# Optimization experiments

Measured on AMD Instinct MI355X. Metric: run time of the kernel, lower is better.

The kernel has to match this reference:

```python
import jax, jax.numpy as jnp
import numpy as np


def setup_inputs() -> dict:
    key = jax.random.key(0)
    k1, k2 = jax.random.split(key)
    latents = jax.random.normal(k1, (32, 1024, 64), dtype=jnp.float32)
    codebook = jax.random.normal(k2, (8192, 64), dtype=jnp.float32)
    return {"latents": latents, "codebook": codebook}


def reference(latents, codebook):
    # Faithful to: cdist(latents_flat, codebook) -> argmin(dim=1) -> reshape(B, L)
    B, L, D = latents.shape
    x = latents.reshape(-1, D)                         # (N, D)
    x2 = jnp.sum(x * x, axis=1, keepdims=True)         # (N, 1)
    c2 = jnp.sum(codebook * codebook, axis=1)          # (K,)
    # (N, K) distance matrix, then argmin reduction
    d2 = x2 - 2.0 * (x @ codebook.T) + c2[None, :]
    indices = jnp.argmin(d2, axis=1)                   # (N,)
    return indices.reshape(B, L)
```

## Files before the change

kernel.cpp:

```cpp
#include <hip/hip_runtime.h>
#include <stdint.h>


#define N_TOTAL 32768
#define K_CODES 8192
#define EPS_GAP 0.008f

typedef __attribute__((ext_vector_type(4)))  float  floatx4;
typedef __attribute__((ext_vector_type(8)))  __bf16 bf16x8;

#define O_C2    0u
#define O_CBSW  32768u
#define O_PS1   2129920u
#define O_PS2   2654208u
#define O_PI1   3178496u
#define O_CNT   3702784u
#define O_LIST  3703040u
#define O_SLOT  3834112u
#define WS_NEED 4096256u

__device__ __forceinline__ unsigned int fkey(float s) {
    unsigned int u = __float_as_uint(s);
    return (u & 0x80000000u) ? ~u : (u | 0x80000000u);
}

__device__ __forceinline__ void load_lds16(const void* g, void* l) {
    __builtin_amdgcn_global_load_lds(
        (const __attribute__((address_space(1))) unsigned int*)g,
        (__attribute__((address_space(3))) unsigned int*)l, 16, 0, 0);
}

__global__ __launch_bounds__(256) void vq_prep(
    const float4* __restrict__ cb, uint4* __restrict__ cbSw,
    float* __restrict__ c2, int* __restrict__ cnt) {
    __shared__ float red[256];
    const int m = threadIdx.x & 31, g = threadIdx.x >> 5;
    const int rb = blockIdx.x;
    if (rb == 0 && threadIdx.x == 0) *cnt = 0;
    float4 a = cb[(size_t)(rb * 32 + m) * 16 + g * 2];
    float4 b = cb[(size_t)(rb * 32 + m) * 16 + g * 2 + 1];
    float x[8] = {a.x, a.y, a.z, a.w, b.x, b.y, b.z, b.w};
    bf16x8 hv, lv;
    float ss = 0.f;
#pragma unroll
    for (int i = 0; i < 8; ++i) {
        float v  = x[i];
        __bf16 hb = (__bf16)v;
        float r  = v - (float)hb;
        hv[i] = hb;
        lv[i] = (__bf16)r;
        ss += v * v;
    }
    cbSw[(size_t)rb * 512 + g * 32 + m]       = __builtin_bit_cast(uint4, hv);
    cbSw[(size_t)rb * 512 + (8 + g) * 32 + m] = __builtin_bit_cast(uint4, lv);
    red[threadIdx.x] = ss;
    __syncthreads();
    if (threadIdx.x < 32) {
        float s = 0.f;
#pragma unroll
        for (int gg = 0; gg < 8; ++gg) s += red[threadIdx.x + 32 * gg];
        c2[rb * 32 + threadIdx.x] = s;
    }
}

__global__ __launch_bounds__(256, 4) void vq_mfma(
    const float4* __restrict__ lat, const uint4* __restrict__ cbSw,
    const float* __restrict__ c2,
    float* __restrict__ pS1, float* __restrict__ pS2, int* __restrict__ pI1) {
    __shared__ uint4 Bs[2][1024];
    const int tid = threadIdx.x;
    const int wr = tid >> 6, lane = tid & 63;
    const int c16 = lane & 15, h4 = lane >> 4;

    const int q0 = blockIdx.x * 128 + wr * 32 + c16;
    bf16x8 aH[2][2], aL[2][2];
#pragma unroll
    for (int qt = 0; qt < 2; ++qt)
#pragma unroll
    for (int c = 0; c < 2; ++c) {
        float4 v0 = lat[(size_t)(q0 + qt * 16) * 16 + c * 8 + h4 * 2];
        float4 v1 = lat[(size_t)(q0 + qt * 16) * 16 + c * 8 + h4 * 2 + 1];
        float x[8] = {v0.x, v0.y, v0.z, v0.w, v1.x, v1.y, v1.z, v1.w};
#pragma unroll
        for (int j = 0; j < 8; ++j) {
            float v  = x[j];
            __bf16 hb = (__bf16)v;
            aH[qt][c][j] = hb;
            aL[qt][c][j] = (__bf16)(v - (float)hb);
        }
    }

    float t1[2][4], t2[2][4]; int i1[2][4];
#pragma unroll
    for (int qt = 0; qt < 2; ++qt)
#pragma unroll
    for (int r = 0; r < 4; ++r) { t1[qt][r] = -3e38f; t2[qt][r] = -3e38f; i1[qt][r] = 0; }

    const int kBase = blockIdx.y * 2048;
    const uint4* srcBase = cbSw + ((size_t)(kBase >> 5) << 9);
    const float* c2g = c2 + kBase + c16;

    float ccCur[4], ccNxt[4];
#pragma unroll
    for (int T = 0; T < 4; ++T) ccCur[T] = c2g[T * 16];
#pragma unroll
    for (int i = 0; i < 4; ++i)
        load_lds16(&srcBase[wr * 256 + i * 64 + lane], &Bs[0][wr * 256 + i * 64]);
    __syncthreads();

    int cur = 0;
    for (int stage = 0; stage < 32; ++stage) {
        if (stage + 1 < 32) {
            const uint4* sp = srcBase + (size_t)(stage + 1) * 1024;
#pragma unroll
            for (int i = 0; i < 4; ++i)
                load_lds16(&sp[wr * 256 + i * 64 + lane],
                           &Bs[cur ^ 1][wr * 256 + i * 64]);
#pragma unroll
            for (int T = 0; T < 4; ++T)
                ccNxt[T] = c2g[(stage + 1) * 64 + T * 16];
        }

        const int colBase = kBase + stage * 64 + c16;

        __builtin_amdgcn_s_setprio(1);
#pragma unroll
        for (int T = 0; T < 4; ++T) {
            const float nn = -0.5f * ccCur[T];
            const int col = colBase + T * 16;
            const int bb = (T >> 1) * 512 + (T & 1) * 16 + c16 + h4 * 32;
            bf16x8 bH0 = __builtin_bit_cast(bf16x8, Bs[cur][bb]);
            bf16x8 bH1 = __builtin_bit_cast(bf16x8, Bs[cur][bb + 128]);
            bf16x8 bL0 = __builtin_bit_cast(bf16x8, Bs[cur][bb + 256]);
            bf16x8 bL1 = __builtin_bit_cast(bf16x8, Bs[cur][bb + 384]);
#pragma unroll
            for (int qt = 0; qt < 2; ++qt) {
                floatx4 acc = {nn, nn, nn, nn};
                acc = __builtin_amdgcn_mfma_f32_16x16x32_bf16(aH[qt][0], bH0, acc, 0, 0, 0);
                acc = __builtin_amdgcn_mfma_f32_16x16x32_bf16(aH[qt][1], bH1, acc, 0, 0, 0);
                acc = __builtin_amdgcn_mfma_f32_16x16x32_bf16(aL[qt][0], bH0, acc, 0, 0, 0);
                acc = __builtin_amdgcn_mfma_f32_16x16x32_bf16(aL[qt][1], bH1, acc, 0, 0, 0);
                acc = __builtin_amdgcn_mfma_f32_16x16x32_bf16(aH[qt][0], bL0, acc, 0, 0, 0);
                acc = __builtin_amdgcn_mfma_f32_16x16x32_bf16(aH[qt][1], bL1, acc, 0, 0, 0);
#pragma unroll
                for (int r = 0; r < 4; ++r) {
                    float a = acc[r];
                    bool gt = a > t1[qt][r];
                    t2[qt][r] = __builtin_amdgcn_fmed3f(a, t1[qt][r], t2[qt][r]);
                    t1[qt][r] = fmaxf(t1[qt][r], a);
                    i1[qt][r] = gt ? col : i1[qt][r];
                }
            }
        }
        __builtin_amdgcn_s_setprio(0);

        __syncthreads();
#pragma unroll
        for (int T = 0; T < 4; ++T) ccCur[T] = ccNxt[T];
        cur ^= 1;
    }

#pragma unroll
    for (int mask = 1; mask <= 8; mask <<= 1) {
#pragma unroll
        for (int qt = 0; qt < 2; ++qt)
#pragma unroll
        for (int r = 0; r < 4; ++r) {
            float o1 = __shfl_xor(t1[qt][r], mask);
            float o2 = __shfl_xor(t2[qt][r], mask);
            int   oi = __shfl_xor(i1[qt][r], mask);
            float n2 = fmaxf(fmaxf(t2[qt][r], o2), fminf(t1[qt][r], o1));
            bool take = (o1 > t1[qt][r]) || (o1 == t1[qt][r] && oi < i1[qt][r]);
            t1[qt][r] = take ? o1 : t1[qt][r];
            i1[qt][r] = take ? oi : i1[qt][r];
            t2[qt][r] = n2;
        }
    }

    if (c16 == 0) {
        const int o0 = blockIdx.y * N_TOTAL;
#pragma unroll
        for (int qt = 0; qt < 2; ++qt) {
            const int qb = blockIdx.x * 128 + wr * 32 + qt * 16 + h4 * 4;
#pragma unroll
            for (int r = 0; r < 4; ++r) {
                pS1[o0 + qb + r] = -2.f * t1[qt][r];
                pS2[o0 + qb + r] = -2.f * t2[qt][r];
                pI1[o0 + qb + r] = i1[qt][r];
            }
        }
    }
}

__global__ void vq_merge4(const float* __restrict__ pS1, const float* __restrict__ pS2,
                          const int* __restrict__ pI1, int* __restrict__ out,
                          int* __restrict__ cnt, int* __restrict__ list,
                          unsigned long long* __restrict__ slot) {
    int q = blockIdx.x * 128 + threadIdx.x;
    float g1 = 3e38f, g2 = 3e38f;
    int   gi = 0x7FFFFFFF;
    float s2v[4];
#pragma unroll
    for (int p = 0; p < 4; ++p) {
        float s1p = pS1[p * N_TOTAL + q];
        float s2p = pS2[p * N_TOTAL + q];
        int   i1p = pI1[p * N_TOTAL + q];
        s2v[p] = s2p;
        bool take = (s1p < g1) || (s1p == g1 && i1p < gi);
        g2 = fminf(g2, fminf(s2p, take ? g1 : s1p));
        if (take) { g1 = s1p; gi = i1p; }
    }
    out[q] = gi;
    if (g2 - g1 < EPS_GAP) {
        int msk = 0;
#pragma unroll
        for (int p = 0; p < 4; ++p)
            if (s2v[p] - g1 < EPS_GAP) msk |= (1 << p);
        int e = atomicAdd(cnt, 1);
        list[e] = q | (msk << 16);
        slot[e] = 0xFFFFFFFFFFFFFFFFull;
    }
}

__global__ __launch_bounds__(256) void vq_exact3(
    const float4* __restrict__ lat, const float* __restrict__ cbf,
    const float* __restrict__ c2, const int* __restrict__ pI1,
    const int* __restrict__ cnt, const int* __restrict__ list,
    unsigned long long* __restrict__ slot) {
    __shared__ float qv[4][64];
    const int n = *cnt;
    const int total = n * 4;
    const int wInB = threadIdx.x >> 6;
    const int lane = threadIdx.x & 63;

    for (int base = blockIdx.x * 4; base < total; base += gridDim.x * 4) {
        const int u = base + wInB;
        const bool act = u < total;
        int e = 0, p = 0, q = 0, msk = 0;
        if (act) {
            e = u >> 2; p = u & 3;
            int v = list[e]; q = v & 0xFFFF; msk = v >> 16;
        }
        __syncthreads();
        if (act && lane < 16) {
            float4 vv = lat[(size_t)q * 16 + lane];
            *(float4*)&qv[wInB][lane * 4] = vv;
        }
        __syncthreads();
        if (act) {
            unsigned long long pk;
            if ((msk >> p) & 1) {
                float best = 3e38f; int bi = 0;
                const int kb = p * 2048;
                for (int i = 0; i < 32; ++i) {
                    const int k = kb + i * 64 + lane;
                    float dot = 0.f;
                    const float4* cp = (const float4*)&cbf[(size_t)k * 64];
#pragma unroll
                    for (int d4 = 0; d4 < 16; ++d4) {
                        float4 cv = cp[d4];
                        dot += qv[wInB][d4 * 4 + 0] * cv.x + qv[wInB][d4 * 4 + 1] * cv.y
                             + qv[wInB][d4 * 4 + 2] * cv.z + qv[wInB][d4 * 4 + 3] * cv.w;
                    }
                    float s = c2[k] - 2.f * dot;
                    if (s < best) { best = s; bi = k; }
                }
                pk = ((unsigned long long)fkey(best) << 32) | (unsigned)bi;
#pragma unroll
                for (int mask = 1; mask <= 32; mask <<= 1) {
                    unsigned long long o = __shfl_xor(pk, mask);
                    pk = o < pk ? o : pk;
                }
            } else {
                const int k = pI1[p * N_TOTAL + q];
                float prod = qv[wInB][lane] * cbf[(size_t)k * 64 + lane];
#pragma unroll
                for (int mask = 1; mask <= 32; mask <<= 1)
                    prod += __shfl_xor(prod, mask);
                float s = c2[k] - 2.f * prod;
                pk = ((unsigned long long)fkey(s) << 32) | (unsigned)k;
            }
            if (lane == 0) atomicMin(&slot[e], pk);
        }
    }
}

__global__ void vq_write(const int* __restrict__ cnt, const int* __restrict__ list,
                         const unsigned long long* __restrict__ slot,
                         int* __restrict__ out) {
    int t = blockIdx.x * 256 + threadIdx.x;
    if (t < *cnt) out[list[t] & 0xFFFF] = (int)(slot[t] & 0xFFFFFFFFull);
}

#define BM 128
#define BN 128
#define PAD 68

__global__ void vq_norms_fb(const float4* __restrict__ cb, float* __restrict__ c2) {
    int t = blockIdx.x * 256 + threadIdx.x;
    int r = t >> 2, p = t & 3;
    float s = 0.f;
#pragma unroll
    for (int i = 0; i < 4; ++i) {
        float4 v = cb[r * 16 + p * 4 + i];
        s += v.x * v.x + v.y * v.y + v.z * v.z + v.w * v.w;
    }
    s += __shfl_xor(s, 1);
    s += __shfl_xor(s, 2);
    if (p == 0) c2[r] = s;
}

__global__ __launch_bounds__(256) void vq_fp32(
    const float4* __restrict__ lat, const float4* __restrict__ cb,
    const float* __restrict__ c2, int ktPer,
    int* __restrict__ outIdx, float* __restrict__ partS, int* __restrict__ partI,
    int writePartial) {
    __shared__ float As[BM][PAD];
    __shared__ float Bsf[BN][PAD];
    __shared__ float c2s[BN];
    const int tid = threadIdx.x;
    const int tx = tid & 15;
    const int ty = tid >> 4;
    const int nBase = blockIdx.x * BM;
    const int kt0 = blockIdx.y * ktPer;
    const int ktN = kt0 + ktPer;
#pragma unroll
    for (int r = 0; r < 8; ++r) {
        int f = tid + 256 * r;
        int mm = f >> 4, d4 = f & 15;
        float4 v = lat[(size_t)(nBase + mm) * 16 + d4];
        *(float4*)&As[mm][d4 * 4] = v;
    }
    float best[8]; int bidx[8];
#pragma unroll
    for (int ii = 0; ii < 8; ++ii) { best[ii] = 3e38f; bidx[ii] = 0; }
    for (int kt = kt0; kt < ktN; ++kt) {
        const int kbase = kt * BN;
        __syncthreads();
#pragma unroll
        for (int r = 0; r < 8; ++r) {
            int f = tid + 256 * r;
            int k = f >> 4, d4 = f & 15;
            float4 v = cb[(size_t)(kbase + k) * 16 + d4];
            *(float4*)&Bsf[k][d4 * 4] = v;
        }
        if (tid < BN) c2s[tid] = c2[kbase + tid];
        __syncthreads();
        float acc[8][8];
#pragma unroll
        for (int ii = 0; ii < 8; ++ii)
#pragma unroll
            for (int jj = 0; jj < 8; ++jj) acc[ii][jj] = 0.f;
#pragma unroll 4
        for (int d4 = 0; d4 < 16; ++d4) {
            float4 a[8], b[8];
#pragma unroll
            for (int ii = 0; ii < 8; ++ii) a[ii] = *(const float4*)&As[tx + 16 * ii][d4 * 4];
#pragma unroll
            for (int jj = 0; jj < 8; ++jj) b[jj] = *(const float4*)&Bsf[ty + 16 * jj][d4 * 4];
#pragma unroll
            for (int ii = 0; ii < 8; ++ii)
#pragma unroll
                for (int jj = 0; jj < 8; ++jj)
                    acc[ii][jj] += a[ii].x * b[jj].x + a[ii].y * b[jj].y
                                 + a[ii].z * b[jj].z + a[ii].w * b[jj].w;
        }
#pragma unroll
        for (int jj = 0; jj < 8; ++jj) {
            int k = kbase + ty + 16 * jj;
            float cc = c2s[ty + 16 * jj];
#pragma unroll
            for (int ii = 0; ii < 8; ++ii) {
                float s = cc - 2.f * acc[ii][jj];
                if (s < best[ii]) { best[ii] = s; bidx[ii] = k; }
            }
        }
    }
    __syncthreads();
    float* redS = &As[0][0];
    int*   redI = (int*)&Bsf[0][0];
#pragma unroll
    for (int ii = 0; ii < 8; ++ii) {
        int mm = tx + 16 * ii;
        redS[ty * BM + mm] = best[ii];
        redI[ty * BM + mm] = bidx[ii];
    }
    __syncthreads();
    if (tid < BM) {
        int mm = tid;
        float bs = redS[mm]; int bi = redI[mm];
#pragma unroll
        for (int t = 1; t < 16; ++t) {
            float s = redS[t * BM + mm]; int i = redI[t * BM + mm];
            if (s < bs || (s == bs && i < bi)) { bs = s; bi = i; }
        }
        int n = nBase + mm;
        if (writePartial) { partS[blockIdx.y * N_TOTAL + n] = bs; partI[blockIdx.y * N_TOTAL + n] = bi; }
        else outIdx[n] = bi;
    }
}

__global__ void vq_merge_fb(const float* __restrict__ partS, const int* __restrict__ partI,
                            int* __restrict__ out) {
    int n = blockIdx.x * 256 + threadIdx.x;
    float s0 = partS[n], s1 = partS[N_TOTAL + n];
    int   i0 = partI[n], i1 = partI[N_TOTAL + n];
    out[n] = (s1 < s0) ? i1 : i0;
}

extern "C" void kernel_launch(void* const* d_in, const int* in_sizes, int n_in,
                              void* d_out, int out_size, void* d_ws, size_t ws_size,
                              hipStream_t stream) {
    const float4* lat = (const float4*)d_in[0];
    const float4* cb  = (const float4*)d_in[1];
    int* out = (int*)d_out;
    char* ws = (char*)d_ws;

    if (ws_size >= WS_NEED) {
        float* c2   = (float*)(ws + O_C2);
        uint4* cbSw = (uint4*)(ws + O_CBSW);
        float* pS1  = (float*)(ws + O_PS1);
        float* pS2  = (float*)(ws + O_PS2);
        int*   pI1  = (int*)(ws + O_PI1);
        int*   cnt  = (int*)(ws + O_CNT);
        int*   list = (int*)(ws + O_LIST);
        unsigned long long* slot = (unsigned long long*)(ws + O_SLOT);

        vq_prep<<<256, 256, 0, stream>>>(cb, cbSw, c2, cnt);
        vq_mfma<<<dim3(256, 4), 256, 0, stream>>>(lat, cbSw, c2, pS1, pS2, pI1);
        vq_merge4<<<256, 128, 0, stream>>>(pS1, pS2, pI1, out, cnt, list, slot);
        vq_exact3<<<1024, 256, 0, stream>>>(lat, (const float*)cb, c2, pI1, cnt, list, slot);
        vq_write<<<128, 256, 0, stream>>>(cnt, list, slot, out);
    } else {
        float* c2 = (float*)ws;
        vq_norms_fb<<<128, 256, 0, stream>>>(cb, c2);
        const size_t needSplit = 32768u + 2u * N_TOTAL * 4u + 2u * N_TOTAL * 4u + 64u;
        if (ws_size >= needSplit) {
            float* partS = (float*)(ws + 32768);
            int*   partI = (int*)(ws + 32768 + 2 * N_TOTAL * 4);
            dim3 grid(N_TOTAL / BM, 2);
            vq_fp32<<<grid, 256, 0, stream>>>(lat, cb, c2, (K_CODES / BN) / 2, out, partS, partI, 1);
            vq_merge_fb<<<N_TOTAL / 256, 256, 0, stream>>>(partS, partI, out);
        } else {
            dim3 grid(N_TOTAL / BM, 1);
            vq_fp32<<<grid, 256, 0, stream>>>(lat, cb, c2, K_CODES / BN, out, nullptr, nullptr, 0);
        }
    }
}
```

Measured before the change: 205.4 us.

## Fuse merge, exact rescoring and writeback into one block-local tail kernel

Replaces the three-kernel tail (merge of partial top-2 results, global-list exact fp32 rescoring, scatter writeback) with a single kernel. Each block merges 128 queries, collects ambiguous queries in a shared-memory list, then rescans the flagged codebook quarters in fp32 with all 256 threads and writes the result directly. This removes two launches and the global atomics, list and slot buffers. The trade-off is that ambiguous queries are processed serially inside each block, which can leave load imbalanced when some blocks have many flagged queries.

```diff
diff --git a/kernel.cpp b/kernel.cpp
--- a/kernel.cpp
+++ b/kernel.cpp
@@ -14,15 +14,7 @@
 #define O_PS1   2129920u
 #define O_PS2   2654208u
 #define O_PI1   3178496u
-#define O_CNT   3702784u
-#define O_LIST  3703040u
-#define O_SLOT  3834112u
 #define WS_NEED 4096256u
-
-__device__ __forceinline__ unsigned int fkey(float s) {
-    unsigned int u = __float_as_uint(s);
-    return (u & 0x80000000u) ? ~u : (u | 0x80000000u);
-}
 
 __device__ __forceinline__ void load_lds16(const void* g, void* l) {
     __builtin_amdgcn_global_load_lds(
@@ -32,11 +24,10 @@
 
 __global__ __launch_bounds__(256) void vq_prep(
     const float4* __restrict__ cb, uint4* __restrict__ cbSw,
-    float* __restrict__ c2, int* __restrict__ cnt) {
+    float* __restrict__ c2) {
     __shared__ float red[256];
     const int m = threadIdx.x & 31, g = threadIdx.x >> 5;
     const int rb = blockIdx.x;
-    if (rb == 0 && threadIdx.x == 0) *cnt = 0;
     float4 a = cb[(size_t)(rb * 32 + m) * 16 + g * 2];
     float4 b = cb[(size_t)(rb * 32 + m) * 16 + g * 2 + 1];
     float x[8] = {a.x, a.y, a.z, a.w, b.x, b.y, b.z, b.w};
@@ -192,104 +183,105 @@
     }
 }
 
-__global__ void vq_merge4(const float* __restrict__ pS1, const float* __restrict__ pS2,
-                          const int* __restrict__ pI1, int* __restrict__ out,
-                          int* __restrict__ cnt, int* __restrict__ list,
-                          unsigned long long* __restrict__ slot) {
-    int q = blockIdx.x * 128 + threadIdx.x;
-    float g1 = 3e38f, g2 = 3e38f;
-    int   gi = 0x7FFFFFFF;
-    float s2v[4];
-#pragma unroll
-    for (int p = 0; p < 4; ++p) {
-        float s1p = pS1[p * N_TOTAL + q];
-        float s2p = pS2[p * N_TOTAL + q];
-        int   i1p = pI1[p * N_TOTAL + q];
-        s2v[p] = s2p;
-        bool take = (s1p < g1) || (s1p == g1 && i1p < gi);
-        g2 = fminf(g2, fminf(s2p, take ? g1 : s1p));
-        if (take) { g1 = s1p; gi = i1p; }
-    }
-    out[q] = gi;
-    if (g2 - g1 < EPS_GAP) {
-        int msk = 0;
-#pragma unroll
-        for (int p = 0; p < 4; ++p)
-            if (s2v[p] - g1 < EPS_GAP) msk |= (1 << p);
-        int e = atomicAdd(cnt, 1);
-        list[e] = q | (msk << 16);
-        slot[e] = 0xFFFFFFFFFFFFFFFFull;
-    }
-}
-
-__global__ __launch_bounds__(256) void vq_exact3(
+__global__ __launch_bounds__(256) void vq_tail(
     const float4* __restrict__ lat, const float* __restrict__ cbf,
-    const float* __restrict__ c2, const int* __restrict__ pI1,
-    const int* __restrict__ cnt, const int* __restrict__ list,
-    unsigned long long* __restrict__ slot) {
-    __shared__ float qv[4][64];
-    const int n = *cnt;
-    const int total = n * 4;
-    const int wInB = threadIdx.x >> 6;
-    const int lane = threadIdx.x & 63;
-
-    for (int base = blockIdx.x * 4; base < total; base += gridDim.x * 4) {
-        const int u = base + wInB;
-        const bool act = u < total;
-        int e = 0, p = 0, q = 0, msk = 0;
-        if (act) {
-            e = u >> 2; p = u & 3;
-            int v = list[e]; q = v & 0xFFFF; msk = v >> 16;
-        }
-        __syncthreads();
-        if (act && lane < 16) {
-            float4 vv = lat[(size_t)q * 16 + lane];
-            *(float4*)&qv[wInB][lane * 4] = vv;
-        }
-        __syncthreads();
-        if (act) {
-            unsigned long long pk;
-            if ((msk >> p) & 1) {
-                float best = 3e38f; int bi = 0;
-                const int kb = p * 2048;
-                for (int i = 0; i < 32; ++i) {
-                    const int k = kb + i * 64 + lane;
-                    float dot = 0.f;
-                    const float4* cp = (const float4*)&cbf[(size_t)k * 64];
-#pragma unroll
-                    for (int d4 = 0; d4 < 16; ++d4) {
-                        float4 cv = cp[d4];
-                        dot += qv[wInB][d4 * 4 + 0] * cv.x + qv[wInB][d4 * 4 + 1] * cv.y
-                             + qv[wInB][d4 * 4 + 2] * cv.z + qv[wInB][d4 * 4 + 3] * cv.w;
-                    }
-                    float s = c2[k] - 2.f * dot;
-                    if (s < best) { best = s; bi = k; }
+    const float* __restrict__ c2,
+    const float* __restrict__ pS1, const float* __restrict__ pS2,
+    const int* __restrict__ pI1, int* __restrict__ out) {
+    __shared__ unsigned char fqv[132];
+    __shared__ unsigned char fmk[132];
+    __shared__ int fcnt;
+    __shared__ float qv[64];
+    __shared__ float redS[256];
+    __shared__ int   redI[256];
+
+    const int tid = threadIdx.x;
+    if (tid == 0) fcnt = 0;
+    __syncthreads();
+
+    if (tid < 128) {
+        const int q = blockIdx.x * 128 + tid;
+        float g1 = 3e38f, g2 = 3e38f;
+        int   gi = 0x7FFFFFFF;
+        float s2v[4];
+#pragma unroll
+        for (int p = 0; p < 4; ++p) {
+            float s1p = pS1[p * N_TOTAL + q];
+            float s2p = pS2[p * N_TOTAL + q];
+            int   i1p = pI1[p * N_TOTAL + q];
+            s2v[p] = s2p;
+            bool take = (s1p < g1) || (s1p == g1 && i1p < gi);
+            g2 = fminf(g2, fminf(s2p, take ? g1 : s1p));
+            if (take) { g1 = s1p; gi = i1p; }
+        }
+        out[q] = gi;
+        if (g2 - g1 < EPS_GAP) {
+            int msk = 0;
+#pragma unroll
+            for (int p = 0; p < 4; ++p)
+                if (s2v[p] - g1 < EPS_GAP) msk |= (1 << p);
+            int e = atomicAdd(&fcnt, 1);
+            fqv[e] = (unsigned char)tid;
+            fmk[e] = (unsigned char)msk;
+        }
+    }
+    __syncthreads();
+
+    const int ne = fcnt;
+    for (int e = 0; e < ne; ++e) {
+        const int lq = fqv[e];
+        const int gq = blockIdx.x * 128 + lq;
+        const int msk = fmk[e];
+        if (tid < 16) {
+            float4 v = lat[(size_t)gq * 16 + tid];
+            *(float4*)&qv[tid * 4] = v;
+        }
+        __syncthreads();
+
+        float best = 3e38f; int bi = 0x7FFFFFFF;
+        if (tid < 4 && !((msk >> tid) & 1)) {
+            const int k = pI1[tid * N_TOTAL + gq];
+            const float4* cp = (const float4*)&cbf[(size_t)k * 64];
+            float dot = 0.f;
+#pragma unroll
+            for (int d4 = 0; d4 < 16; ++d4) {
+                float4 cv = cp[d4];
+                dot += qv[d4 * 4 + 0] * cv.x + qv[d4 * 4 + 1] * cv.y
+                     + qv[d4 * 4 + 2] * cv.z + qv[d4 * 4 + 3] * cv.w;
+            }
+            float s = c2[k] - 2.f * dot;
+            if (s < best || (s == best && k < bi)) { best = s; bi = k; }
+        }
+#pragma unroll
+        for (int p = 0; p < 4; ++p) if ((msk >> p) & 1) {
+            for (int j = tid; j < 2048; j += 256) {
+                const int k = p * 2048 + j;
+                const float4* cp = (const float4*)&cbf[(size_t)k * 64];
+                float dot = 0.f;
+#pragma unroll
+                for (int d4 = 0; d4 < 16; ++d4) {
+                    float4 cv = cp[d4];
+                    dot += qv[d4 * 4 + 0] * cv.x + qv[d4 * 4 + 1] * cv.y
+                         + qv[d4 * 4 + 2] * cv.z + qv[d4 * 4 + 3] * cv.w;
                 }
-                pk = ((unsigned long long)fkey(best) << 32) | (unsigned)bi;
-#pragma unroll
-                for (int mask = 1; mask <= 32; mask <<= 1) {
-                    unsigned long long o = __shfl_xor(pk, mask);
-                    pk = o < pk ? o : pk;
+                float s = c2[k] - 2.f * dot;
+                if (s < best || (s == best && k < bi)) { best = s; bi = k; }
+            }
+        }
+        redS[tid] = best; redI[tid] = bi;
+        __syncthreads();
+        for (int s = 128; s > 0; s >>= 1) {
+            if (tid < s) {
+                float os = redS[tid + s]; int oi = redI[tid + s];
+                if (os < redS[tid] || (os == redS[tid] && oi < redI[tid])) {
+                    redS[tid] = os; redI[tid] = oi;
                 }
-            } else {
-                const int k = pI1[p * N_TOTAL + q];
-                float prod = qv[wInB][lane] * cbf[(size_t)k * 64 + lane];
-#pragma unroll
-                for (int mask = 1; mask <= 32; mask <<= 1)
-                    prod += __shfl_xor(prod, mask);
-                float s = c2[k] - 2.f * prod;
-                pk = ((unsigned long long)fkey(s) << 32) | (unsigned)k;
-            }
-            if (lane == 0) atomicMin(&slot[e], pk);
-        }
-    }
-}
-
-__global__ void vq_write(const int* __restrict__ cnt, const int* __restrict__ list,
-                         const unsigned long long* __restrict__ slot,
-                         int* __restrict__ out) {
-    int t = blockIdx.x * 256 + threadIdx.x;
-    if (t < *cnt) out[list[t] & 0xFFFF] = (int)(slot[t] & 0xFFFFFFFFull);
+            }
+            __syncthreads();
+        }
+        if (tid == 0) out[gq] = redI[0];
+        __syncthreads();
+    }
 }
 
 #define BM 128
@@ -422,15 +414,10 @@
         float* pS1  = (float*)(ws + O_PS1);
         float* pS2  = (float*)(ws + O_PS2);
         int*   pI1  = (int*)(ws + O_PI1);
-        int*   cnt  = (int*)(ws + O_CNT);
-        int*   list = (int*)(ws + O_LIST);
-        unsigned long long* slot = (unsigned long long*)(ws + O_SLOT);
-
-        vq_prep<<<256, 256, 0, stream>>>(cb, cbSw, c2, cnt);
+
+        vq_prep<<<256, 256, 0, stream>>>(cb, cbSw, c2);
         vq_mfma<<<dim3(256, 4), 256, 0, stream>>>(lat, cbSw, c2, pS1, pS2, pI1);
-        vq_merge4<<<256, 128, 0, stream>>>(pS1, pS2, pI1, out, cnt, list, slot);
-        vq_exact3<<<1024, 256, 0, stream>>>(lat, (const float*)cb, c2, pI1, cnt, list, slot);
-        vq_write<<<128, 256, 0, stream>>>(cnt, list, slot, out);
+        vq_tail<<<256, 256, 0, stream>>>(lat, (const float*)cb, c2, pS1, pS2, pI1, out);
     } else {
         float* c2 = (float*)ws;
         vq_norms_fb<<<128, 256, 0, stream>>>(cb, c2);
```

Measured after the change: 195.1 us. 1.05x faster.
